# Kernel tuning notes

Hardware: AMD Instinct MI355X
Metric: run time of the kernel (lower is better)

The kernel has to match this reference:

```python
import jax, jax.numpy as jnp
import numpy as np

ALPHA = 3.0   # config.model.hgnn_alpha
K = 16        # config.model.k_neighbors
S, N, E, D = 3, 8192, 1024, 512


def setup_inputs() -> dict:
    key = jax.random.key(0)
    k1, k2, k3 = jax.random.split(key, 3)
    x = jax.random.normal(k1, (1,), dtype=jnp.float32)  # only used for device in torch
    node_embed = jax.random.normal(k2, (S, N, D), dtype=jnp.float32)  # embednod tables
    edge_embed = jax.random.normal(k3, (S, E, D), dtype=jnp.float32)  # embedhy tables
    return {"x": x, "node_embed": node_embed, "edge_embed": edge_embed}


def reference(x, node_embed, edge_embed):
    # sim[s] = n_embed @ h_embed.T  -> [S, N, E]
    sim = jnp.einsum('snd,sed->sne', node_embed, edge_embed)
    # adj = softmax(relu(alpha * sim), dim=1 over hyperedges)
    adj = jax.nn.softmax(jax.nn.relu(ALPHA * sim), axis=-1)
    # top-k mask along hyperedge axis (scatter 1s at top-k indices per row)
    _, topk_idx = jax.lax.top_k(adj, K)  # [S, N, K]
    s_idx = jnp.arange(S)[:, None, None]
    n_idx = jnp.arange(N)[None, :, None]
    mask = jnp.zeros_like(adj).at[s_idx, n_idx, topk_idx].set(1.0)
    adj = adj * mask
    # hard threshold: binary incidence matrix per scale.
    # Original then drops all-zero hyperedge columns and returns nonzero
    # (node_idx, hyperedge_idx) pairs -- data-dependent shapes, so the dense
    # binary incidence [S, N, E] is the jit-compatible equivalent output;
    # the index lists are exactly its nonzero coordinates.
    hard = jnp.where(adj > 0.5, 1.0, 0.0)
    return hard
```

## Files before the change

### kernel.cpp

```cpp
#include <hip/hip_runtime.h>
#include <cmath>

#define SS 3
#define NN 8192
#define EE 1024
#define DD 512
#define ALPHA 3.0f
#define TAU 0.03f

typedef __attribute__((ext_vector_type(8))) short bf16x8;
typedef __attribute__((ext_vector_type(4))) float f32x4;

#define AS1(p) ((const __attribute__((address_space(1))) void*)(p))
#define AS3(p) ((__attribute__((address_space(3))) void*)(p))

__device__ __forceinline__ unsigned short f2bf(float x) {
    unsigned u = __float_as_uint(x);
    return (unsigned short)((u + 0x7fffu + ((u >> 16) & 1u)) >> 16);
}
__device__ __forceinline__ float bf2f(unsigned short h) {
    return __uint_as_float(((unsigned)h) << 16);
}

__device__ __forceinline__ void gload_lds16(const unsigned short* g, unsigned short* l) {
    __builtin_amdgcn_global_load_lds(AS1(g), AS3(l), 16, 0, 0);
}

__global__ __launch_bounds__(256)
void split_bf16_kernel(const float* __restrict__ in,
                       unsigned short* __restrict__ hi,
                       unsigned short* __restrict__ lo, int n4)
{
    int i = blockIdx.x * blockDim.x + threadIdx.x;
    if (i >= n4) return;
    float4 v = ((const float4*)in)[i];
    ushort4 h, l;
    h.x = f2bf(v.x); l.x = f2bf(v.x - bf2f(h.x));
    h.y = f2bf(v.y); l.y = f2bf(v.y - bf2f(h.y));
    h.z = f2bf(v.z); l.z = f2bf(v.z - bf2f(h.z));
    h.w = f2bf(v.w); l.w = f2bf(v.w - bf2f(h.w));
    ((ushort4*)hi)[i] = h;
    ((ushort4*)lo)[i] = l;
}

__global__ __launch_bounds__(256)
void gemm_mfma_kernel(const unsigned short* __restrict__ Ah,
                      const unsigned short* __restrict__ Al,
                      const unsigned short* __restrict__ Bh,
                      const unsigned short* __restrict__ Bl,
                      float* __restrict__ out)
{
    const int s  = blockIdx.z;
    const int m0 = blockIdx.y * 128;
    const int n0 = blockIdx.x * 128;

    const unsigned short* pAh = Ah + (size_t)s * NN * DD;
    const unsigned short* pAl = Al + (size_t)s * NN * DD;
    const unsigned short* pBh = Bh + (size_t)s * EE * DD;
    const unsigned short* pBl = Bl + (size_t)s * EE * DD;
    float* C = out + (size_t)s * NN * EE;

    __shared__ unsigned short lds[4 * 128 * 32];

    const int t    = threadIdx.x;
    const int lane = t & 63;
    const int wid  = t >> 6;
    const int wm   = wid >> 1;
    const int wn   = wid & 1;
    const int fr   = lane & 15;
    const int kg   = lane >> 4;

    f32x4 acc[4][4];
#pragma unroll
    for (int i = 0; i < 4; ++i)
#pragma unroll
        for (int j = 0; j < 4; ++j) acc[i][j] = (f32x4){0.f, 0.f, 0.f, 0.f};

    for (int k0 = 0; k0 < DD; k0 += 32) {
#pragma unroll
        for (int i = 0; i < 2; ++i) {
            const int c   = i * 256 + t;
            const int row = c >> 2;
            const int kp  = (c & 3) * 8;
            const size_t ga = (size_t)(m0 + row) * DD + k0 + kp;
            const size_t gb = (size_t)(n0 + row) * DD + k0 + kp;
            gload_lds16(pAh + ga, &lds[0 * 4096 + c * 8]);
            gload_lds16(pAl + ga, &lds[1 * 4096 + c * 8]);
            gload_lds16(pBh + gb, &lds[2 * 4096 + c * 8]);
            gload_lds16(pBl + gb, &lds[3 * 4096 + c * 8]);
        }
        __syncthreads();

        bf16x8 ah[4], al[4], bh[4], bl[4];
#pragma unroll
        for (int i = 0; i < 4; ++i) {
            const int r = wm * 64 + i * 16 + fr;
            ah[i] = *(const bf16x8*)&lds[0 * 4096 + r * 32 + kg * 8];
            al[i] = *(const bf16x8*)&lds[1 * 4096 + r * 32 + kg * 8];
        }
#pragma unroll
        for (int j = 0; j < 4; ++j) {
            const int r = wn * 64 + j * 16 + fr;
            bh[j] = *(const bf16x8*)&lds[2 * 4096 + r * 32 + kg * 8];
            bl[j] = *(const bf16x8*)&lds[3 * 4096 + r * 32 + kg * 8];
        }
#pragma unroll
        for (int i = 0; i < 4; ++i)
#pragma unroll
            for (int j = 0; j < 4; ++j) {
                acc[i][j] = __builtin_amdgcn_mfma_f32_16x16x32_bf16(ah[i], bh[j], acc[i][j], 0, 0, 0);
                acc[i][j] = __builtin_amdgcn_mfma_f32_16x16x32_bf16(ah[i], bl[j], acc[i][j], 0, 0, 0);
                acc[i][j] = __builtin_amdgcn_mfma_f32_16x16x32_bf16(al[i], bh[j], acc[i][j], 0, 0, 0);
            }
        __syncthreads();
    }

#pragma unroll
    for (int i = 0; i < 4; ++i)
#pragma unroll
        for (int j = 0; j < 4; ++j) {
            const int col = n0 + wn * 64 + j * 16 + fr;
#pragma unroll
            for (int r = 0; r < 4; ++r) {
                const int row = m0 + wm * 64 + i * 16 + kg * 4 + r;
                C[(size_t)row * EE + col] = fmaxf(ALPHA * acc[i][j][r], 0.f);
            }
        }
}

__global__ void zero_count_kernel(int* __restrict__ count) {
    if (threadIdx.x == 0 && blockIdx.x == 0) count[0] = 0;
}

__global__ __launch_bounds__(256)
void softmax_threshold_flag_kernel(float* __restrict__ out,
                                   int* __restrict__ count,
                                   int* __restrict__ worklist)
{
    const int wave = threadIdx.x >> 6;
    const int lane = threadIdx.x & 63;
    const size_t row = (size_t)blockIdx.x * 4 + wave;
    float* p = out + row * EE;

    float z[16];
    float m = 0.f;
#pragma unroll
    for (int j = 0; j < 4; ++j) {
        float4 v = *(const float4*)(p + j * 256 + lane * 4);
        z[j*4+0] = v.x; z[j*4+1] = v.y; z[j*4+2] = v.z; z[j*4+3] = v.w;
        m = fmaxf(m, fmaxf(fmaxf(v.x, v.y), fmaxf(v.z, v.w)));
    }
#pragma unroll
    for (int off = 32; off >= 1; off >>= 1)
        m = fmaxf(m, __shfl_xor(m, off, 64));

    float e[16];
    float sum = 0.f;
#pragma unroll
    for (int j = 0; j < 16; ++j) {
        e[j] = expf(z[j] - m);
        sum += e[j];
    }
#pragma unroll
    for (int off = 32; off >= 1; off >>= 1)
        sum += __shfl_xor(sum, off, 64);

    const float thr = 0.5f * sum;
    const float T   = m + logf(thr);
    int lf = 0;
#pragma unroll
    for (int j = 0; j < 16; ++j)
        lf |= (fabsf(z[j] - T) < TAU) ? 1 : 0;

#pragma unroll
    for (int j = 0; j < 4; ++j) {
        float4 o;
        o.x = (e[j*4+0] > thr) ? 1.f : 0.f;
        o.y = (e[j*4+1] > thr) ? 1.f : 0.f;
        o.z = (e[j*4+2] > thr) ? 1.f : 0.f;
        o.w = (e[j*4+3] > thr) ? 1.f : 0.f;
        *(float4*)(p + j * 256 + lane * 4) = o;
    }
    const int anyf = __any(lf);
    if (anyf && lane == 0) {
        int idx = atomicAdd(count, 1);
        worklist[idx] = (int)row;
    }
}

__global__ __launch_bounds__(256)
void fixup_z_kernel(const float* __restrict__ node, const float* __restrict__ edge,
                    const int* __restrict__ count, const int* __restrict__ worklist,
                    float* __restrict__ zbuf, int zcap)
{
    __shared__ float sa[DD];
    const int t    = threadIdx.x;
    const int lane = t & 63;
    const int wid  = t >> 6;

    int nwork = count[0];
    if (nwork > zcap) nwork = zcap;
    const int items = nwork * 4;

    for (int item = blockIdx.x; item < items; item += gridDim.x) {
        const int w   = item >> 2;
        const int row = worklist[w];
        const int c0  = (item & 3) * 256;
        const int s   = row / NN;
        const float* a = node + (size_t)row * DD;
        const float* B = edge + (size_t)s * EE * DD;

        __syncthreads();
        if (t < DD / 4) ((float4*)sa)[t] = ((const float4*)a)[t];
        __syncthreads();

        const float4 va0 = ((const float4*)sa)[lane];
        const float4 va1 = ((const float4*)sa)[64 + lane];

        const int cbase = c0 + wid * 64;
        for (int g = 0; g < 16; ++g) {
            float acc[4];
#pragma unroll
            for (int j = 0; j < 4; ++j) {
                const float* b = B + (size_t)(cbase + g * 4 + j) * DD;
                float4 b0 = *(const float4*)(b + lane * 4);
                float4 b1 = *(const float4*)(b + 256 + lane * 4);
                float av;
                av = va0.x * b0.x;
                av = fmaf(va0.y, b0.y, av);
                av = fmaf(va0.z, b0.z, av);
                av = fmaf(va0.w, b0.w, av);
                av = fmaf(va1.x, b1.x, av);
                av = fmaf(va1.y, b1.y, av);
                av = fmaf(va1.z, b1.z, av);
                av = fmaf(va1.w, b1.w, av);
                acc[j] = av;
            }
#pragma unroll
            for (int off = 32; off >= 1; off >>= 1) {
#pragma unroll
                for (int j = 0; j < 4; ++j)
                    acc[j] += __shfl_xor(acc[j], off, 64);
            }
            if (lane == 0) {
#pragma unroll
                for (int j = 0; j < 4; ++j)
                    zbuf[(size_t)w * EE + cbase + g * 4 + j] = fmaxf(ALPHA * acc[j], 0.f);
            }
        }
    }
}

__global__ __launch_bounds__(256)
void fixup_finish_kernel(const float* __restrict__ zbuf,
                         const int* __restrict__ count, const int* __restrict__ worklist,
                         float* __restrict__ out, int zcap)
{
    const int lane = threadIdx.x & 63;
    const int wid  = threadIdx.x >> 6;
    int nwork = count[0];
    if (nwork > zcap) nwork = zcap;

    for (int w = blockIdx.x * 4 + wid; w < nwork; w += gridDim.x * 4) {
        const int row = worklist[w];
        const float* p = zbuf + (size_t)w * EE;

        float z[16];
        float m = 0.f;
#pragma unroll
        for (int j = 0; j < 4; ++j) {
            float4 v = *(const float4*)(p + j * 256 + lane * 4);
            z[j*4+0] = v.x; z[j*4+1] = v.y; z[j*4+2] = v.z; z[j*4+3] = v.w;
            m = fmaxf(m, fmaxf(fmaxf(v.x, v.y), fmaxf(v.z, v.w)));
        }
#pragma unroll
        for (int off = 32; off >= 1; off >>= 1)
            m = fmaxf(m, __shfl_xor(m, off, 64));

        float e[16], sum = 0.f;
#pragma unroll
        for (int j = 0; j < 16; ++j) { e[j] = expf(z[j] - m); sum += e[j]; }
#pragma unroll
        for (int off = 32; off >= 1; off >>= 1)
            sum += __shfl_xor(sum, off, 64);

        const float thr = 0.5f * sum;
        float* q = out + (size_t)row * EE;
#pragma unroll
        for (int j = 0; j < 4; ++j) {
            float4 o;
            o.x = (e[j*4+0] > thr) ? 1.f : 0.f;
            o.y = (e[j*4+1] > thr) ? 1.f : 0.f;
            o.z = (e[j*4+2] > thr) ? 1.f : 0.f;
            o.w = (e[j*4+3] > thr) ? 1.f : 0.f;
            *(float4*)(q + j * 256 + lane * 4) = o;
        }
    }
}

__global__ __launch_bounds__(256)
void fixup2_kernel(const float* __restrict__ node, const float* __restrict__ edge,
                   const int* __restrict__ count, const int* __restrict__ worklist,
                   float* __restrict__ out, int start)
{
    __shared__ float sa[DD];
    __shared__ float zrow[EE];
    __shared__ float red[8];

    const int t    = threadIdx.x;
    const int lane = t & 63;
    const int wid  = t >> 6;
    const int nwork = count[0];

    for (int w = start + blockIdx.x; w < nwork; w += gridDim.x) {
        const int row = worklist[w];
        const int s = row / NN;
        const float* a = node + (size_t)row * DD;
        const float* B = edge + (size_t)s * EE * DD;

        __syncthreads();
        if (t < DD / 4) ((float4*)sa)[t] = ((const float4*)a)[t];
        __syncthreads();

        float4 va0 = ((const float4*)sa)[lane];
        float4 va1 = ((const float4*)sa)[64 + lane];

        for (int c = wid; c < EE; c += 4) {
            const float* b = B + (size_t)c * DD;
            float4 b0 = *(const float4*)(b + lane * 4);
            float4 b1 = *(const float4*)(b + 256 + lane * 4);
            float acc;
            acc = va0.x * b0.x;
            acc = fmaf(va0.y, b0.y, acc);
            acc = fmaf(va0.z, b0.z, acc);
            acc = fmaf(va0.w, b0.w, acc);
            acc = fmaf(va1.x, b1.x, acc);
            acc = fmaf(va1.y, b1.y, acc);
            acc = fmaf(va1.z, b1.z, acc);
            acc = fmaf(va1.w, b1.w, acc);
#pragma unroll
            for (int off = 32; off >= 1; off >>= 1)
                acc += __shfl_xor(acc, off, 64);
            if (lane == 0) zrow[c] = fmaxf(ALPHA * acc, 0.f);
        }
        __syncthreads();

        float z[4], m = 0.f;
#pragma unroll
        for (int j = 0; j < 4; ++j) {
            z[j] = zrow[j * 256 + t];
            m = fmaxf(m, z[j]);
        }
#pragma unroll
        for (int off = 32; off >= 1; off >>= 1)
            m = fmaxf(m, __shfl_xor(m, off, 64));
        if (lane == 0) red[wid] = m;
        __syncthreads();
        m = fmaxf(fmaxf(red[0], red[1]), fmaxf(red[2], red[3]));

        float e[4], sum = 0.f;
#pragma unroll
        for (int j = 0; j < 4; ++j) { e[j] = expf(z[j] - m); sum += e[j]; }
#pragma unroll
        for (int off = 32; off >= 1; off >>= 1)
            sum += __shfl_xor(sum, off, 64);
        if (lane == 0) red[4 + wid] = sum;
        __syncthreads();
        sum = red[4] + red[5] + red[6] + red[7];

        const float thr = 0.5f * sum;
#pragma unroll
        for (int j = 0; j < 4; ++j)
            out[(size_t)row * EE + j * 256 + t] = (e[j] > thr) ? 1.f : 0.f;
        __syncthreads();
    }
}

#define BM 128
#define BN 128
#define BK 16
#define TM 8
#define TN 8

__global__ __launch_bounds__(256, 2)
void gemm_relu_kernel(const float* __restrict__ node,
                      const float* __restrict__ edge,
                      float* __restrict__ out)
{
    const int s  = blockIdx.z;
    const int m0 = blockIdx.y * BM;
    const int n0 = blockIdx.x * BN;

    const float* A = node + (size_t)s * NN * DD;
    const float* B = edge + (size_t)s * EE * DD;
    float*       C = out  + (size_t)s * NN * EE;

    __shared__ float As[BK][BM + 4];
    __shared__ float Bs[BK][BN + 4];

    const int tid = threadIdx.x;
    const int tx  = tid % 16;
    const int ty  = tid / 16;
    const int lrow = tid / 4;
    const int lcol = (tid % 4) * 4;

    float acc[TM][TN];
#pragma unroll
    for (int i = 0; i < TM; ++i)
#pragma unroll
        for (int j = 0; j < TN; ++j) acc[i][j] = 0.f;

    for (int k0 = 0; k0 < DD; k0 += BK) {
#pragma unroll
        for (int p = 0; p < 2; ++p) {
            const int r = lrow + p * 64;
            float4 v = *(const float4*)(A + (size_t)(m0 + r) * DD + k0 + lcol);
            As[lcol + 0][r] = v.x; As[lcol + 1][r] = v.y;
            As[lcol + 2][r] = v.z; As[lcol + 3][r] = v.w;
            float4 w = *(const float4*)(B + (size_t)(n0 + r) * DD + k0 + lcol);
            Bs[lcol + 0][r] = w.x; Bs[lcol + 1][r] = w.y;
            Bs[lcol + 2][r] = w.z; Bs[lcol + 3][r] = w.w;
        }
        __syncthreads();
#pragma unroll
        for (int k = 0; k < BK; ++k) {
            float a[TM], b[TN];
            float4 a0 = *(const float4*)&As[k][ty * 8];
            float4 a1 = *(const float4*)&As[k][ty * 8 + 4];
            a[0]=a0.x; a[1]=a0.y; a[2]=a0.z; a[3]=a0.w;
            a[4]=a1.x; a[5]=a1.y; a[6]=a1.z; a[7]=a1.w;
            float4 b0 = *(const float4*)&Bs[k][tx * 8];
            float4 b1 = *(const float4*)&Bs[k][tx * 8 + 4];
            b[0]=b0.x; b[1]=b0.y; b[2]=b0.z; b[3]=b0.w;
            b[4]=b1.x; b[5]=b1.y; b[6]=b1.z; b[7]=b1.w;
#pragma unroll
            for (int i = 0; i < TM; ++i)
#pragma unroll
                for (int j = 0; j < TN; ++j)
                    acc[i][j] = fmaf(a[i], b[j], acc[i][j]);
        }
        __syncthreads();
    }
#pragma unroll
    for (int i = 0; i < TM; ++i) {
        const size_t row = (size_t)(m0 + ty * 8 + i);
        float4 o0, o1;
        o0.x = fmaxf(ALPHA * acc[i][0], 0.f);
        o0.y = fmaxf(ALPHA * acc[i][1], 0.f);
        o0.z = fmaxf(ALPHA * acc[i][2], 0.f);
        o0.w = fmaxf(ALPHA * acc[i][3], 0.f);
        o1.x = fmaxf(ALPHA * acc[i][4], 0.f);
        o1.y = fmaxf(ALPHA * acc[i][5], 0.f);
        o1.z = fmaxf(ALPHA * acc[i][6], 0.f);
        o1.w = fmaxf(ALPHA * acc[i][7], 0.f);
        *(float4*)(C + row * EE + n0 + tx * 8)     = o0;
        *(float4*)(C + row * EE + n0 + tx * 8 + 4) = o1;
    }
}

__global__ __launch_bounds__(256)
void softmax_threshold_kernel(float* __restrict__ out)
{
    const int wave = threadIdx.x >> 6;
    const int lane = threadIdx.x & 63;
    const size_t row = (size_t)blockIdx.x * 4 + wave;
    float* p = out + row * EE;

    float z[16];
    float m = 0.f;
#pragma unroll
    for (int j = 0; j < 4; ++j) {
        float4 v = *(const float4*)(p + j * 256 + lane * 4);
        z[j*4+0] = v.x; z[j*4+1] = v.y; z[j*4+2] = v.z; z[j*4+3] = v.w;
        m = fmaxf(m, fmaxf(fmaxf(v.x, v.y), fmaxf(v.z, v.w)));
    }
#pragma unroll
    for (int off = 32; off >= 1; off >>= 1)
        m = fmaxf(m, __shfl_xor(m, off, 64));
    float e[16], sum = 0.f;
#pragma unroll
    for (int j = 0; j < 16; ++j) { e[j] = expf(z[j] - m); sum += e[j]; }
#pragma unroll
    for (int off = 32; off >= 1; off >>= 1)
        sum += __shfl_xor(sum, off, 64);
    const float thr = 0.5f * sum;
#pragma unroll
    for (int j = 0; j < 4; ++j) {
        float4 o;
        o.x = (e[j*4+0] > thr) ? 1.f : 0.f;
        o.y = (e[j*4+1] > thr) ? 1.f : 0.f;
        o.z = (e[j*4+2] > thr) ? 1.f : 0.f;
        o.w = (e[j*4+3] > thr) ? 1.f : 0.f;
        *(float4*)(p + j * 256 + lane * 4) = o;
    }
}

extern "C" void kernel_launch(void* const* d_in, const int* in_sizes, int n_in,
                              void* d_out, int out_size, void* d_ws, size_t ws_size,
                              hipStream_t stream) {
    const float* node = (const float*)d_in[1];
    const float* edge = (const float*)d_in[2];
    float* out = (float*)d_out;

    const size_t SAe = (size_t)SS * NN * DD;
    const size_t SBe = (size_t)SS * EE * DD;
    const size_t split_bytes = (2 * SAe + 2 * SBe) * 2;
    const size_t wl_bytes    = (size_t)(SS * NN + 1) * 4;
    const size_t base_need   = split_bytes + wl_bytes;

    if (ws_size >= base_need) {
        unsigned short* Ah = (unsigned short*)d_ws;
        unsigned short* Al = Ah + SAe;
        unsigned short* Bh = Al + SAe;
        unsigned short* Bl = Bh + SBe;
        int* count    = (int*)(Bl + SBe);
        int* worklist = count + 1;

        const size_t zoff = (base_need + 255) & ~(size_t)255;
        int zcap = 0;
        if (ws_size > zoff) {
            size_t zc = (ws_size - zoff) / ((size_t)EE * 4);
            zcap = (int)(zc > 4096 ? 4096 : zc);
        }
        float* zbuf = (float*)((char*)d_ws + zoff);

        split_bf16_kernel<<<(int)(SAe / 4 + 255) / 256, 256, 0, stream>>>(node, Ah, Al, (int)(SAe / 4));
        split_bf16_kernel<<<(int)(SBe / 4 + 255) / 256, 256, 0, stream>>>(edge, Bh, Bl, (int)(SBe / 4));

        zero_count_kernel<<<1, 64, 0, stream>>>(count);

        dim3 g1(EE / 128, NN / 128, SS);
        gemm_mfma_kernel<<<g1, 256, 0, stream>>>(Ah, Al, Bh, Bl, out);

        softmax_threshold_flag_kernel<<<(SS * NN) / 4, 256, 0, stream>>>(out, count, worklist);

        if (zcap > 0) {
            fixup_z_kernel<<<1024, 256, 0, stream>>>(node, edge, count, worklist, zbuf, zcap);
            fixup_finish_kernel<<<64, 256, 0, stream>>>(zbuf, count, worklist, out, zcap);
        }
        fixup2_kernel<<<512, 256, 0, stream>>>(node, edge, count, worklist, out, zcap);
    } else {
        dim3 g1(EE / BN, NN / BM, SS);
        gemm_relu_kernel<<<g1, 256, 0, stream>>>(node, edge, out);
        softmax_threshold_kernel<<<(SS * NN) / 4, 256, 0, stream>>>(out);
    }
}
```

Baseline: 161.5 us.

## Swizzle GEMM LDS layout, swap block raster order, merge split kernels

Interleaves the hi/lo bf16 halves of each row into a single 64-element LDS row and XOR-swizzles the 16-byte slots by row, so the fragment reads avoid LDS bank conflicts. Swaps the grid axes so consecutive blocks walk the node (M) dimension while sharing an edge tile, which changes L2 reuse of the B operand. Merges the two bf16 split launches into one kernel to cut a launch. The load loop now issues eight gloads per thread with per-element branching on the source pointer.

Measured after the change: 151.2 us. 1.07x faster.

```diff
diff --git a/kernel.cpp b/kernel.cpp
--- a/kernel.cpp
+++ b/kernel.cpp
@@ -27,20 +27,33 @@
 }
 
 __global__ __launch_bounds__(256)
-void split_bf16_kernel(const float* __restrict__ in,
-                       unsigned short* __restrict__ hi,
-                       unsigned short* __restrict__ lo, int n4)
-{
+void split_both_kernel(const float* __restrict__ node, const float* __restrict__ edge,
+                       unsigned short* __restrict__ Ah, unsigned short* __restrict__ Al,
+                       unsigned short* __restrict__ Bh, unsigned short* __restrict__ Bl)
+{
+    const int nA = SS * NN * DD / 4;
+    const int nB = SS * EE * DD / 4;
     int i = blockIdx.x * blockDim.x + threadIdx.x;
-    if (i >= n4) return;
-    float4 v = ((const float4*)in)[i];
+
+    const float4* src;
+    unsigned short* hi;
+    unsigned short* lo;
+    int idx;
+    if (i < nA) {
+        src = (const float4*)node; hi = Ah; lo = Al; idx = i;
+    } else if (i < nA + nB) {
+        src = (const float4*)edge; hi = Bh; lo = Bl; idx = i - nA;
+    } else {
+        return;
+    }
+    float4 v = src[idx];
     ushort4 h, l;
     h.x = f2bf(v.x); l.x = f2bf(v.x - bf2f(h.x));
     h.y = f2bf(v.y); l.y = f2bf(v.y - bf2f(h.y));
     h.z = f2bf(v.z); l.z = f2bf(v.z - bf2f(h.z));
     h.w = f2bf(v.w); l.w = f2bf(v.w - bf2f(h.w));
-    ((ushort4*)hi)[i] = h;
-    ((ushort4*)lo)[i] = l;
+    ((ushort4*)hi)[idx] = h;
+    ((ushort4*)lo)[idx] = l;
 }
 
 __global__ __launch_bounds__(256)
@@ -51,8 +64,8 @@
                       float* __restrict__ out)
 {
     const int s  = blockIdx.z;
-    const int m0 = blockIdx.y * 128;
-    const int n0 = blockIdx.x * 128;
+    const int m0 = blockIdx.x * 128;
+    const int n0 = blockIdx.y * 128;
 
     const unsigned short* pAh = Ah + (size_t)s * NN * DD;
     const unsigned short* pAl = Al + (size_t)s * NN * DD;
@@ -60,7 +73,7 @@
     const unsigned short* pBl = Bl + (size_t)s * EE * DD;
     float* C = out + (size_t)s * NN * EE;
 
-    __shared__ unsigned short lds[4 * 128 * 32];
+    __shared__ unsigned short lds[2 * 1024 * 8];
 
     const int t    = threadIdx.x;
     const int lane = t & 63;
@@ -78,16 +91,21 @@
 
     for (int k0 = 0; k0 < DD; k0 += 32) {
 #pragma unroll
-        for (int i = 0; i < 2; ++i) {
-            const int c   = i * 256 + t;
-            const int row = c >> 2;
-            const int kp  = (c & 3) * 8;
-            const size_t ga = (size_t)(m0 + row) * DD + k0 + kp;
-            const size_t gb = (size_t)(n0 + row) * DD + k0 + kp;
-            gload_lds16(pAh + ga, &lds[0 * 4096 + c * 8]);
-            gload_lds16(pAl + ga, &lds[1 * 4096 + c * 8]);
-            gload_lds16(pBh + gb, &lds[2 * 4096 + c * 8]);
-            gload_lds16(pBl + gb, &lds[3 * 4096 + c * 8]);
+        for (int i = 0; i < 8; ++i) {
+            const int c    = i * 256 + t;
+            const int pc   = c & 1023;
+            const int row  = pc >> 3;
+            const int slot = pc & 7;
+            const int j    = slot ^ (row & 7);
+            const unsigned short* src;
+            if (c < 1024) {
+                src = (j < 4) ? pAh + (size_t)(m0 + row) * DD + k0 + j * 8
+                              : pAl + (size_t)(m0 + row) * DD + k0 + (j - 4) * 8;
+            } else {
+                src = (j < 4) ? pBh + (size_t)(n0 + row) * DD + k0 + j * 8
+                              : pBl + (size_t)(n0 + row) * DD + k0 + (j - 4) * 8;
+            }
+            gload_lds16(src, &lds[c * 8]);
         }
         __syncthreads();
 
@@ -95,14 +113,14 @@
 #pragma unroll
         for (int i = 0; i < 4; ++i) {
             const int r = wm * 64 + i * 16 + fr;
-            ah[i] = *(const bf16x8*)&lds[0 * 4096 + r * 32 + kg * 8];
-            al[i] = *(const bf16x8*)&lds[1 * 4096 + r * 32 + kg * 8];
+            ah[i] = *(const bf16x8*)&lds[r * 64 + ((kg)     ^ (r & 7)) * 8];
+            al[i] = *(const bf16x8*)&lds[r * 64 + ((4 + kg) ^ (r & 7)) * 8];
         }
 #pragma unroll
         for (int j = 0; j < 4; ++j) {
             const int r = wn * 64 + j * 16 + fr;
-            bh[j] = *(const bf16x8*)&lds[2 * 4096 + r * 32 + kg * 8];
-            bl[j] = *(const bf16x8*)&lds[3 * 4096 + r * 32 + kg * 8];
+            bh[j] = *(const bf16x8*)&lds[8192 + r * 64 + ((kg)     ^ (r & 7)) * 8];
+            bl[j] = *(const bf16x8*)&lds[8192 + r * 64 + ((4 + kg) ^ (r & 7)) * 8];
         }
 #pragma unroll
         for (int i = 0; i < 4; ++i)
@@ -524,12 +542,12 @@
         }
         float* zbuf = (float*)((char*)d_ws + zoff);
 
-        split_bf16_kernel<<<(int)(SAe / 4 + 255) / 256, 256, 0, stream>>>(node, Ah, Al, (int)(SAe / 4));
-        split_bf16_kernel<<<(int)(SBe / 4 + 255) / 256, 256, 0, stream>>>(edge, Bh, Bl, (int)(SBe / 4));
+        const int n4 = (int)((SAe + SBe) / 4);
+        split_both_kernel<<<(n4 + 255) / 256, 256, 0, stream>>>(node, edge, Ah, Al, Bh, Bl);
 
         zero_count_kernel<<<1, 64, 0, stream>>>(count);
 
-        dim3 g1(EE / 128, NN / 128, SS);
+        dim3 g1(NN / 128, EE / 128, SS);
         gemm_mfma_kernel<<<g1, 256, 0, stream>>>(Ah, Al, Bh, Bl, out);
 
         softmax_threshold_flag_kernel<<<(SS * NN) / 4, 256, 0, stream>>>(out, count, worklist);
```
